# Optimization experiments

Hardware: AMD Instinct MI355X
Metric: run time of the kernel (lower is better)

## Reference

```python
import jax, jax.numpy as jnp
import numpy as np

H = 64            # hidden_dim
N_NODES = 100000
N_EDGES = 2000000
IN_DIM = 2 * H + 2  # src_emb || dst_emb || src_fiedler || dst_fiedler


def setup_inputs() -> dict:
    key = jax.random.key(0)
    ks = jax.random.split(key, 10)
    node_embeddings = jax.random.normal(ks[0], (N_NODES, H), dtype=jnp.float32)
    edge_index = jax.random.randint(ks[1], (2, N_EDGES), 0, N_NODES, dtype=jnp.int64)
    fiedler_vector = jax.random.normal(ks[2], (N_NODES,), dtype=jnp.float32)
    # MLP scorer params: Linear(130,64)+ReLU, Linear(64,64)+ReLU, Linear(64,1)
    def lin(k, fan_in, fan_out):
        bound = 1.0 / np.sqrt(fan_in)
        kw, kb = jax.random.split(k)
        W = jax.random.uniform(kw, (fan_in, fan_out), jnp.float32, -bound, bound)
        b = jax.random.uniform(kb, (fan_out,), jnp.float32, -bound, bound)
        return W, b
    W1, b1 = lin(ks[3], IN_DIM, H)
    W2, b2 = lin(ks[4], H, H)
    W3, b3 = lin(ks[5], H, 1)
    return {
        "node_embeddings": node_embeddings,
        "fiedler_vector": fiedler_vector,
        "W1": W1, "b1": b1, "W2": W2, "b2": b2, "W3": W3, "b3": b3,
        "edge_index": edge_index,
        "num_nodes": N_NODES,
    }


def reference(node_embeddings, fiedler_vector, W1, b1, W2, b2, W3, b3, edge_index, num_nodes):
    src, dst = edge_index[0], edge_index[1]
    # Gather + concat edge features: [E, 2H+2]
    feats = jnp.concatenate(
        [
            node_embeddings[src],               # [E, H]
            node_embeddings[dst],               # [E, H]
            fiedler_vector[src][:, None],        # [E, 1]
            fiedler_vector[dst][:, None],        # [E, 1]
        ],
        axis=-1,
    )
    # Edge scorer MLP (Dropout is identity in eval mode)
    h = jax.nn.relu(feats @ W1 + b1)
    h = jax.nn.relu(h @ W2 + b2)
    edge_scores = (h @ W3 + b3)[:, 0]  # [E]
    return edge_scores
```

## Files before the change

### kernel.cpp

```cpp
#include <hip/hip_runtime.h>


#define HD 64

typedef __attribute__((ext_vector_type(8))) _Float16 half8;
typedef __attribute__((ext_vector_type(8))) short  short8;
typedef __attribute__((ext_vector_type(8))) float  float8;
typedef __attribute__((ext_vector_type(4))) float  f32x4;

__device__ __forceinline__ half8 relu_h8(half8 x) {
    short8 b = __builtin_bit_cast(short8, x);
    short8 m = b >> 15;
    b = b & ~m;
    return __builtin_bit_cast(half8, b);
}

__global__ __launch_bounds__(256) void precompute_uv(
    const float* __restrict__ emb, const float* __restrict__ fied,
    const float* __restrict__ W1, const float* __restrict__ b1,
    _Float16* __restrict__ u, _Float16* __restrict__ v,
    int n_nodes, int ntiles)
{
    const int lane = threadIdx.x & 63;
    const int q = lane >> 4;
    const int c = lane & 15;
    const int wid = blockIdx.x * (blockDim.x >> 6) + (threadIdx.x >> 6);
    const int nw  = gridDim.x * (blockDim.x >> 6);

    half8 Bf[8][2];
    #pragma unroll
    for (int t = 0; t < 8; ++t)
        #pragma unroll
        for (int ks = 0; ks < 2; ++ks)
            #pragma unroll
            for (int j = 0; j < 8; ++j) {
                int k = q * 8 + j + 32 * ks;
                int row = (t < 4) ? k : (64 + k);
                Bf[t][ks][j] = (_Float16)W1[row * HD + (t & 3) * 16 + c];
            }
    float b1f[4], wsf[4], wdf[4];
    #pragma unroll
    for (int t = 0; t < 4; ++t) {
        b1f[t] = b1[t * 16 + c];
        wsf[t] = W1[128 * HD + t * 16 + c];
        wdf[t] = W1[129 * HD + t * 16 + c];
    }

    for (int tile = wid; tile < ntiles; tile += nw) {
        const int n0 = tile * 16;
        int na = n0 + c;
        if (na >= n_nodes) na = n_nodes - 1;
        const float* rp = emb + (size_t)na * HD + q * 8;
        float8 a0 = *(const float8*)rp;
        float8 a1 = *(const float8*)(rp + 32);
        half8 A0 = __builtin_convertvector(a0, half8);
        half8 A1 = __builtin_convertvector(a1, half8);

        f32x4 aU[4] = {}, aV[4] = {};
        #pragma unroll
        for (int t = 0; t < 4; ++t) {
            aU[t] = __builtin_amdgcn_mfma_f32_16x16x32_f16(A0, Bf[t][0],     aU[t], 0, 0, 0);
            aU[t] = __builtin_amdgcn_mfma_f32_16x16x32_f16(A1, Bf[t][1],     aU[t], 0, 0, 0);
            aV[t] = __builtin_amdgcn_mfma_f32_16x16x32_f16(A0, Bf[4 + t][0], aV[t], 0, 0, 0);
            aV[t] = __builtin_amdgcn_mfma_f32_16x16x32_f16(A1, Bf[4 + t][1], aV[t], 0, 0, 0);
        }

        float fv[4];
        #pragma unroll
        for (int r = 0; r < 4; ++r) {
            int n = n0 + q * 4 + r;
            fv[r] = (n < n_nodes) ? fied[n] : 0.f;
        }
        #pragma unroll
        for (int t = 0; t < 4; ++t)
            #pragma unroll
            for (int r = 0; r < 4; ++r) {
                int n = n0 + q * 4 + r;
                if (n < n_nodes) {
                    u[(size_t)n * HD + t * 16 + c] =
                        (_Float16)(aU[t][r] + b1f[t] + fv[r] * wsf[t]);
                    v[(size_t)n * HD + t * 16 + c] =
                        (_Float16)(aV[t][r] + fv[r] * wdf[t]);
                }
            }
    }
}

__global__ __launch_bounds__(256) void edge_mlp(
    const _Float16* __restrict__ u, const _Float16* __restrict__ v,
    const int* __restrict__ src, const int* __restrict__ dst,
    const float* __restrict__ W2, const float* __restrict__ b2,
    const float* __restrict__ W3, const float* __restrict__ b3,
    float* __restrict__ out, int E, int ntiles)
{
    const int lane = threadIdx.x & 63;
    const int q = lane >> 4;
    const int c = lane & 15;
    const int wid = blockIdx.x * (blockDim.x >> 6) + (threadIdx.x >> 6);
    const int nw  = gridDim.x * (blockDim.x >> 6);

    half8 Af[4][2];
    #pragma unroll
    for (int t = 0; t < 4; ++t)
        #pragma unroll
        for (int ks = 0; ks < 2; ++ks)
            #pragma unroll
            for (int j = 0; j < 8; ++j) {
                int k = q * 8 + j + 32 * ks;
                Af[t][ks][j] = (_Float16)W2[k * HD + t * 16 + c];
            }
    float b2q[4][4], w3q[4][4];
    #pragma unroll
    for (int t = 0; t < 4; ++t)
        #pragma unroll
        for (int r = 0; r < 4; ++r) {
            int f = t * 16 + q * 4 + r;
            b2q[t][r] = b2[f];
            w3q[t][r] = W3[f];
        }
    const float b3v = b3[0];

    int tile = wid;
    half8 Ua, Ub, Va, Vb;
    if (tile < ntiles) {
        int e = tile * 16 + c; if (e >= E) e = E - 1;
        const int s = src[e], d = dst[e];
        const half8* up = (const half8*)(u + (unsigned)s * HD + q * 8);
        const half8* vp = (const half8*)(v + (unsigned)d * HD + q * 8);
        Ua = up[0]; Ub = up[4]; Va = vp[0]; Vb = vp[4];
    }

    for (; tile < ntiles; tile += nw) {
        const int nt = tile + nw;
        int sn = 0, dn = 0;
        if (nt < ntiles) {
            int e2 = nt * 16 + c; if (e2 >= E) e2 = E - 1;
            sn = src[e2]; dn = dst[e2];
        }
        half8 B0 = relu_h8(Ua + Va);
        half8 B1 = relu_h8(Ub + Vb);
        if (nt < ntiles) {
            const half8* up = (const half8*)(u + (unsigned)sn * HD + q * 8);
            const half8* vp = (const half8*)(v + (unsigned)dn * HD + q * 8);
            Ua = up[0]; Ub = up[4]; Va = vp[0]; Vb = vp[4];
        }

        f32x4 acc[4] = {};
        #pragma unroll
        for (int t = 0; t < 4; ++t) {
            acc[t] = __builtin_amdgcn_mfma_f32_16x16x32_f16(Af[t][0], B0, acc[t], 0, 0, 0);
            acc[t] = __builtin_amdgcn_mfma_f32_16x16x32_f16(Af[t][1], B1, acc[t], 0, 0, 0);
        }

        float p = 0.f;
        #pragma unroll
        for (int t = 0; t < 4; ++t)
            #pragma unroll
            for (int r = 0; r < 4; ++r)
                p = fmaf(fmaxf(acc[t][r] + b2q[t][r], 0.f), w3q[t][r], p);
        p += __shfl_xor(p, 16, 64);
        p += __shfl_xor(p, 32, 64);
        if (q == 0) {
            int e = tile * 16 + c;
            if (e < E) out[e] = p + b3v;
        }
    }
}

extern "C" void kernel_launch(void* const* d_in, const int* in_sizes, int n_in,
                              void* d_out, int out_size, void* d_ws, size_t ws_size,
                              hipStream_t stream) {
    const float* emb  = (const float*)d_in[0];
    const float* fied = (const float*)d_in[1];
    const float* W1   = (const float*)d_in[2];
    const float* b1   = (const float*)d_in[3];
    const float* W2   = (const float*)d_in[4];
    const float* b2   = (const float*)d_in[5];
    const float* W3   = (const float*)d_in[6];
    const float* b3   = (const float*)d_in[7];
    const int*   eidx = (const int*)d_in[8];

    const int n_nodes = in_sizes[1];
    const int E       = in_sizes[8] / 2;
    const int* srcp = eidx;
    const int* dstp = eidx + E;

    _Float16* u = (_Float16*)d_ws;
    _Float16* v = u + (size_t)n_nodes * HD;

    const int ntilesN = (n_nodes + 15) / 16;
    precompute_uv<<<512, 256, 0, stream>>>(emb, fied, W1, b1, u, v,
                                           n_nodes, ntilesN);

    const int ntilesE = (E + 15) / 16;
    edge_mlp<<<1024, 256, 0, stream>>>(u, v, srcp, dstp, W2, b2, W3, b3,
                                       (float*)d_out, E, ntilesE);
}
```

Measured before the change: 206.8 us.

## Double-buffer edge gathers two tiles per wave and vectorize node precompute stores

The edge MLP now processes two 16-edge tiles per iteration, keeping two sets of prefetched u/v gathers in flight so that more gather latency is hidden, and the grid is doubled. The node precompute kernel swaps the MFMA operand order so each lane owns one node and writes contiguous half4 chunks instead of scattered scalar half stores, reading the fiedler value once per lane. Per-row biases and weights are loaded as float4 vectors. In exchange, register pressure rises from the extra prefetch buffers, which may lower occupancy.

```diff
diff --git a/kernel.cpp b/kernel.cpp
--- a/kernel.cpp
+++ b/kernel.cpp
@@ -4,6 +4,7 @@
 #define HD 64
 
 typedef __attribute__((ext_vector_type(8))) _Float16 half8;
+typedef __attribute__((ext_vector_type(4))) _Float16 half4;
 typedef __attribute__((ext_vector_type(8))) short  short8;
 typedef __attribute__((ext_vector_type(8))) float  float8;
 typedef __attribute__((ext_vector_type(4))) float  f32x4;
@@ -27,62 +28,59 @@
     const int wid = blockIdx.x * (blockDim.x >> 6) + (threadIdx.x >> 6);
     const int nw  = gridDim.x * (blockDim.x >> 6);
 
-    half8 Bf[8][2];
-    #pragma unroll
-    for (int t = 0; t < 8; ++t)
+    half8 Au[4][2], Av[4][2];
+    #pragma unroll
+    for (int t = 0; t < 4; ++t)
         #pragma unroll
         for (int ks = 0; ks < 2; ++ks)
             #pragma unroll
             for (int j = 0; j < 8; ++j) {
-                int k = q * 8 + j + 32 * ks;
-                int row = (t < 4) ? k : (64 + k);
-                Bf[t][ks][j] = (_Float16)W1[row * HD + (t & 3) * 16 + c];
-            }
-    float b1f[4], wsf[4], wdf[4];
+                int k = ks * 32 + q * 8 + j;
+                Au[t][ks][j] = (_Float16)W1[k * HD + t * 16 + c];
+                Av[t][ks][j] = (_Float16)W1[(64 + k) * HD + t * 16 + c];
+            }
+    f32x4 b1q[4], wsq[4], wdq[4];
     #pragma unroll
     for (int t = 0; t < 4; ++t) {
-        b1f[t] = b1[t * 16 + c];
-        wsf[t] = W1[128 * HD + t * 16 + c];
-        wdf[t] = W1[129 * HD + t * 16 + c];
+        b1q[t] = *(const f32x4*)(b1 + t * 16 + q * 4);
+        wsq[t] = *(const f32x4*)(W1 + 128 * HD + t * 16 + q * 4);
+        wdq[t] = *(const f32x4*)(W1 + 129 * HD + t * 16 + q * 4);
     }
 
     for (int tile = wid; tile < ntiles; tile += nw) {
         const int n0 = tile * 16;
-        int na = n0 + c;
-        if (na >= n_nodes) na = n_nodes - 1;
+        const int n  = n0 + c;
+        int na = n; if (na >= n_nodes) na = n_nodes - 1;
         const float* rp = emb + (size_t)na * HD + q * 8;
         float8 a0 = *(const float8*)rp;
         float8 a1 = *(const float8*)(rp + 32);
-        half8 A0 = __builtin_convertvector(a0, half8);
-        half8 A1 = __builtin_convertvector(a1, half8);
+        half8 B0 = __builtin_convertvector(a0, half8);
+        half8 B1 = __builtin_convertvector(a1, half8);
 
         f32x4 aU[4] = {}, aV[4] = {};
         #pragma unroll
         for (int t = 0; t < 4; ++t) {
-            aU[t] = __builtin_amdgcn_mfma_f32_16x16x32_f16(A0, Bf[t][0],     aU[t], 0, 0, 0);
-            aU[t] = __builtin_amdgcn_mfma_f32_16x16x32_f16(A1, Bf[t][1],     aU[t], 0, 0, 0);
-            aV[t] = __builtin_amdgcn_mfma_f32_16x16x32_f16(A0, Bf[4 + t][0], aV[t], 0, 0, 0);
-            aV[t] = __builtin_amdgcn_mfma_f32_16x16x32_f16(A1, Bf[4 + t][1], aV[t], 0, 0, 0);
-        }
-
-        float fv[4];
-        #pragma unroll
-        for (int r = 0; r < 4; ++r) {
-            int n = n0 + q * 4 + r;
-            fv[r] = (n < n_nodes) ? fied[n] : 0.f;
-        }
-        #pragma unroll
-        for (int t = 0; t < 4; ++t)
+            aU[t] = __builtin_amdgcn_mfma_f32_16x16x32_f16(Au[t][0], B0, aU[t], 0, 0, 0);
+            aU[t] = __builtin_amdgcn_mfma_f32_16x16x32_f16(Au[t][1], B1, aU[t], 0, 0, 0);
+            aV[t] = __builtin_amdgcn_mfma_f32_16x16x32_f16(Av[t][0], B0, aV[t], 0, 0, 0);
+            aV[t] = __builtin_amdgcn_mfma_f32_16x16x32_f16(Av[t][1], B1, aV[t], 0, 0, 0);
+        }
+
+        const float fv = fied[na];
+        const bool ok = (n < n_nodes);
+        #pragma unroll
+        for (int t = 0; t < 4; ++t) {
+            half4 hu, hv;
             #pragma unroll
             for (int r = 0; r < 4; ++r) {
-                int n = n0 + q * 4 + r;
-                if (n < n_nodes) {
-                    u[(size_t)n * HD + t * 16 + c] =
-                        (_Float16)(aU[t][r] + b1f[t] + fv[r] * wsf[t]);
-                    v[(size_t)n * HD + t * 16 + c] =
-                        (_Float16)(aV[t][r] + fv[r] * wdf[t]);
-                }
-            }
+                hu[r] = (_Float16)(aU[t][r] + b1q[t][r] + fv * wsq[t][r]);
+                hv[r] = (_Float16)(aV[t][r] + fv * wdq[t][r]);
+            }
+            if (ok) {
+                *(half4*)(u + (size_t)n * HD + t * 16 + q * 4) = hu;
+                *(half4*)(v + (size_t)n * HD + t * 16 + q * 4) = hv;
+            }
+        }
     }
 }
 
@@ -106,52 +104,40 @@
         for (int ks = 0; ks < 2; ++ks)
             #pragma unroll
             for (int j = 0; j < 8; ++j) {
-                int k = q * 8 + j + 32 * ks;
+                int k = ks * 32 + q * 8 + j;
                 Af[t][ks][j] = (_Float16)W2[k * HD + t * 16 + c];
             }
-    float b2q[4][4], w3q[4][4];
-    #pragma unroll
-    for (int t = 0; t < 4; ++t)
-        #pragma unroll
-        for (int r = 0; r < 4; ++r) {
-            int f = t * 16 + q * 4 + r;
-            b2q[t][r] = b2[f];
-            w3q[t][r] = W3[f];
-        }
+    f32x4 b2q[4], w3q[4];
+    #pragma unroll
+    for (int t = 0; t < 4; ++t) {
+        b2q[t] = *(const f32x4*)(b2 + t * 16 + q * 4);
+        w3q[t] = *(const f32x4*)(W3 + t * 16 + q * 4);
+    }
     const float b3v = b3[0];
 
-    int tile = wid;
-    half8 Ua, Ub, Va, Vb;
-    if (tile < ntiles) {
+    const int stride = nw * 2;
+    int base = wid * 2;
+
+    half8 U0a, U0b, V0a, V0b, U1a, U1b, V1a, V1b;
+
+    auto load_idx = [&](int tile, int& s, int& d) {
         int e = tile * 16 + c; if (e >= E) e = E - 1;
-        const int s = src[e], d = dst[e];
+        s = src[e]; d = dst[e];
+    };
+    auto issue = [&](int s, int d, half8& Ua, half8& Ub, half8& Va, half8& Vb) {
         const half8* up = (const half8*)(u + (unsigned)s * HD + q * 8);
         const half8* vp = (const half8*)(v + (unsigned)d * HD + q * 8);
         Ua = up[0]; Ub = up[4]; Va = vp[0]; Vb = vp[4];
-    }
-
-    for (; tile < ntiles; tile += nw) {
-        const int nt = tile + nw;
-        int sn = 0, dn = 0;
-        if (nt < ntiles) {
-            int e2 = nt * 16 + c; if (e2 >= E) e2 = E - 1;
-            sn = src[e2]; dn = dst[e2];
-        }
+    };
+    auto compute_store = [&](int tile, half8 Ua, half8 Ub, half8 Va, half8 Vb) {
         half8 B0 = relu_h8(Ua + Va);
         half8 B1 = relu_h8(Ub + Vb);
-        if (nt < ntiles) {
-            const half8* up = (const half8*)(u + (unsigned)sn * HD + q * 8);
-            const half8* vp = (const half8*)(v + (unsigned)dn * HD + q * 8);
-            Ua = up[0]; Ub = up[4]; Va = vp[0]; Vb = vp[4];
-        }
-
         f32x4 acc[4] = {};
         #pragma unroll
         for (int t = 0; t < 4; ++t) {
             acc[t] = __builtin_amdgcn_mfma_f32_16x16x32_f16(Af[t][0], B0, acc[t], 0, 0, 0);
             acc[t] = __builtin_amdgcn_mfma_f32_16x16x32_f16(Af[t][1], B1, acc[t], 0, 0, 0);
         }
-
         float p = 0.f;
         #pragma unroll
         for (int t = 0; t < 4; ++t)
@@ -164,6 +150,30 @@
             int e = tile * 16 + c;
             if (e < E) out[e] = p + b3v;
         }
+    };
+
+    if (base < ntiles) {
+        int s, d; load_idx(base, s, d);
+        issue(s, d, U0a, U0b, V0a, V0b);
+    }
+    if (base + 1 < ntiles) {
+        int s, d; load_idx(base + 1, s, d);
+        issue(s, d, U1a, U1b, V1a, V1b);
+    }
+
+    for (; base < ntiles; base += stride) {
+        const int nb = base + stride;
+        const bool h2 = (nb < ntiles), h3 = (nb + 1 < ntiles);
+        int s2 = 0, d2 = 0, s3 = 0, d3 = 0;
+        if (h2) load_idx(nb, s2, d2);
+        if (h3) load_idx(nb + 1, s3, d3);
+
+        compute_store(base, U0a, U0b, V0a, V0b);
+        if (h2) issue(s2, d2, U0a, U0b, V0a, V0b);
+
+        if (base + 1 < ntiles)
+            compute_store(base + 1, U1a, U1b, V1a, V1b);
+        if (h3) issue(s3, d3, U1a, U1b, V1a, V1b);
     }
 }
 
@@ -193,6 +203,6 @@
                                            n_nodes, ntilesN);
 
     const int ntilesE = (E + 15) / 16;
-    edge_mlp<<<1024, 256, 0, stream>>>(u, v, srcp, dstp, W2, b2, W3, b3,
+    edge_mlp<<<2048, 256, 0, stream>>>(u, v, srcp, dstp, W2, b2, W3, b3,
                                        (float*)d_out, E, ntilesE);
 }
```

Result: faster. 181.8 us (-12.1%).
